# Performance work log

Measured on AMD Instinct MI355X. Metric: run time of the kernel, lower is better.

Reference implementation:

```python
import jax, jax.numpy as jnp
import numpy as np

N_NODES = 50000


def _relgraphconv(x, W, Wloop, b, src, dst, etypes, n_nodes):
    # DGL RelGraphConv (regularizer=None, self_loop=True, norm=None):
    # out[i] = sum over incoming edges (j->i, rel r) of W_r @ x[j]  +  W_loop @ x[i]  +  b
    # low-mem form: transform all nodes per relation, then gather per edge.
    h_rel = jnp.einsum('ni,rio->rno', x, W)          # [R, N, out]
    msg = h_rel[etypes, src]                          # [E, out]
    agg = jax.ops.segment_sum(msg, dst, num_segments=n_nodes)  # [N, out]
    return agg + x @ Wloop + b


def setup_inputs() -> dict:
    key = jax.random.key(0)
    ks = jax.random.split(key, 12)
    N, E, n_state = N_NODES, 800000, 128
    inp = {
        'x': jax.random.normal(ks[0], (N, n_state), dtype=jnp.float32),
        'src': jax.random.randint(ks[1], (E,), 0, N, dtype=jnp.int32),
        'dst': jax.random.randint(ks[2], (E,), 0, N, dtype=jnp.int32),
        'etypes': jax.random.randint(ks[3], (E,), 0, 2, dtype=jnp.int32),
        'cell_size': jax.random.randint(ks[4], (N,), 0, 8, dtype=jnp.int32),
        'max_size': jax.random.randint(ks[5], (N,), 0, 8, dtype=jnp.int32),
        'W1': jax.random.normal(ks[6], (2, n_state, 64), dtype=jnp.float32) * 0.05,
        'loop1': jax.random.normal(ks[7], (n_state, 64), dtype=jnp.float32) * 0.05,
        'b1': jnp.zeros((64,), dtype=jnp.float32),
        'W2': jax.random.normal(ks[8], (2, 64, 64), dtype=jnp.float32) * 0.05,
        'loop2': jax.random.normal(ks[9], (64, 64), dtype=jnp.float32) * 0.05,
        'b2': jnp.zeros((64,), dtype=jnp.float32),
        'W3': jax.random.normal(ks[10], (2, 64, 2), dtype=jnp.float32) * 0.05,
        'loop3': jax.random.normal(ks[11], (64, 2), dtype=jnp.float32) * 0.05,
        'b3': jnp.zeros((2,), dtype=jnp.float32),
    }
    return inp


def reference(x, src, dst, etypes, cell_size, max_size,
              W1, loop1, b1, W2, loop2, b2, W3, loop3, b3):
    N = x.shape[0]
    h = jax.nn.relu(_relgraphconv(x, W1, loop1, b1, src, dst, etypes, N))
    h = jax.nn.relu(_relgraphconv(h, W2, loop2, b2, src, dst, etypes, N))
    h = _relgraphconv(h, W3, loop3, b3, src, dst, etypes, N)   # [N, 2]
    # action mask: col 0 = cannot upsize, col 1 = cannot downsize
    upper = cell_size >= (max_size - 1)
    lower = cell_size == 0
    mask = jnp.stack([upper, lower], axis=1)                   # [N, 2] bool
    return jnp.where(mask, h.min() - 1.0, h)
```

## Files before the change

### kernel.cpp

```cpp
#include <hip/hip_runtime.h>


#define STRIDE 64
#define BINCAP 2560

typedef unsigned short ushortT;
typedef __attribute__((ext_vector_type(8))) short short8;
typedef __attribute__((ext_vector_type(4))) float f32x4;

__device__ inline ushortT f2bf(float f) {
    union { float f; unsigned u; } v; v.f = f;
    unsigned r = v.u + 0x7FFFu + ((v.u >> 16) & 1u);
    return (ushortT)(r >> 16);
}
__device__ inline float bf2f(ushortT h) {
    union { unsigned u; float f; } v; v.u = ((unsigned)h) << 16;
    return v.f;
}

__device__ inline void atomicMinF(float* addr, float v) {
    if (v >= 0.f) atomicMin((int*)addr, __float_as_int(v));
    else          atomicMax((unsigned int*)addr, __float_as_uint(v));
}

__global__ __launch_bounds__(256) void pack_init_kernel(
    const float* __restrict__ W1, const float* __restrict__ loop1,
    const float* __restrict__ W2, const float* __restrict__ loop2,
    ushortT* __restrict__ BP1, ushortT* __restrict__ BP2,
    int* __restrict__ bincnt, float* __restrict__ minval,
    int* __restrict__ done, int NBINS) {
    int g = (int)blockIdx.x * 256 + (int)threadIdx.x;
    if (g < NBINS) bincnt[g] = 0;
    if (g == 0) { *(int*)minval = 0x7f7f7f7f; *done = 0; }
    if (g < 3072) {
        int l = g & 63, ks = (g >> 6) & 3, ct = g >> 8;
        int c = ct * 16 + (l & 15);
        int mat = c >> 6, cc = c & 63;
        int kbase = ks * 32 + (l >> 4) * 8;
        ushortT* dstp = BP1 + (size_t)g * 8;
#pragma unroll
        for (int j = 0; j < 8; ++j) {
            int k = kbase + j;
            float v = (mat < 2) ? W1[((size_t)mat * 128 + k) * 64 + cc]
                                : loop1[(size_t)k * 64 + cc];
            dstp[j] = f2bf(v);
        }
    } else {
        int s = g - 3072;
        int l = s & 63, ks = (s >> 6) & 1, ct = s >> 7;
        int c = ct * 16 + (l & 15);
        int mat = c >> 6, cc = c & 63;
        int kbase = ks * 32 + (l >> 4) * 8;
        ushortT* dstp = BP2 + (size_t)s * 8;
#pragma unroll
        for (int j = 0; j < 8; ++j) {
            int k = kbase + j;
            float v = (mat < 2) ? W2[((size_t)mat * 64 + k) * 64 + cc]
                                : loop2[(size_t)k * 64 + cc];
            dstp[j] = f2bf(v);
        }
    }
}

__global__ __launch_bounds__(256) void k1_kernel(
    const float* __restrict__ x, const ushortT* __restrict__ BP1,
    const float* __restrict__ b1,
    ushortT* __restrict__ hrelb, ushortT* __restrict__ H1b,
    const int* __restrict__ src, const int* __restrict__ dst,
    const int* __restrict__ et, int* __restrict__ bincnt, int2* __restrict__ binbuf,
    int N, int E, int NBINS, int NBA) {
    __shared__ int hist[512];
    __shared__ int gbase[512];
    __shared__ ushortT rnk[4096];

    const int t = (int)threadIdx.x;

    if ((int)blockIdx.x < NBA) {
        for (int i = t; i < NBINS; i += 256) hist[i] = 0;
        __syncthreads();
        const int base = (int)blockIdx.x * 4096;
#pragma unroll
        for (int i = 0; i < 16; ++i) {
            int e = base + t + i * 256;
            if (e < E) {
                int bb = dst[e] >> 7;
                rnk[t + i * 256] = (ushortT)atomicAdd(&hist[bb], 1);
            }
        }
        __syncthreads();
        for (int i = t; i < NBINS; i += 256) {
            int h = hist[i];
            gbase[i] = h ? atomicAdd(&bincnt[i], h) : 0;
        }
        __syncthreads();
#pragma unroll
        for (int i = 0; i < 16; ++i) {
            int e = base + t + i * 256;
            if (e < E) {
                int dd = dst[e];
                int bb = dd >> 7;
                int v = et[e] * N + src[e];
                int pos = gbase[bb] + (int)rnk[t + i * 256];
                if (pos < BINCAP)
                    binbuf[(size_t)bb * BINCAP + pos] = make_int2(dd, v);
            }
        }
        return;
    }
    const int w = t >> 6, lane = t & 63;
    const int rowbase = (((int)blockIdx.x - NBA) * 4 + w) * 16;
    const int m = lane & 15, quad = lane >> 4;
    const int nclamp = min(rowbase + m, N - 1);

    short8 a[4];
    const float* xp = x + (size_t)nclamp * 128 + quad * 8;
#pragma unroll
    for (int ks = 0; ks < 4; ++ks) {
        float4 g0 = *(const float4*)(xp + ks * 32);
        float4 g1 = *(const float4*)(xp + ks * 32 + 4);
        a[ks][0] = (short)f2bf(g0.x); a[ks][1] = (short)f2bf(g0.y);
        a[ks][2] = (short)f2bf(g0.z); a[ks][3] = (short)f2bf(g0.w);
        a[ks][4] = (short)f2bf(g1.x); a[ks][5] = (short)f2bf(g1.y);
        a[ks][6] = (short)f2bf(g1.z); a[ks][7] = (short)f2bf(g1.w);
    }

    f32x4 acc[12];
#pragma unroll
    for (int ct = 0; ct < 12; ++ct) acc[ct] = (f32x4){0.f, 0.f, 0.f, 0.f};

#pragma unroll
    for (int ks = 0; ks < 4; ++ks) {
#pragma unroll
        for (int ct = 0; ct < 12; ++ct) {
            short8 b = *(const short8*)&BP1[((size_t)(ct * 4 + ks) * 64 + lane) * 8];
            acc[ct] = __builtin_amdgcn_mfma_f32_16x16x32_bf16(a[ks], b, acc[ct], 0, 0, 0);
        }
    }

    const int node0 = rowbase + quad * 4;
#pragma unroll
    for (int ct = 0; ct < 12; ++ct) {
        int c = ct * 16 + m;
        int mat = c >> 6, cc = c & 63;
        float bias = (mat == 2) ? b1[cc] : 0.f;
#pragma unroll
        for (int j = 0; j < 4; ++j) {
            int n = node0 + j;
            if (n < N) {
                float v = acc[ct][j] + bias;
                if (mat < 2) hrelb[((size_t)mat * N + n) * 64 + cc] = f2bf(v);
                else         H1b[(size_t)n * 64 + cc] = f2bf(v);
            }
        }
    }
}

__global__ __launch_bounds__(512, 4) void ag2_kernel(
    const ushortT* __restrict__ hrelb, const ushortT* __restrict__ H1b,
    const ushortT* __restrict__ BP2, const float* __restrict__ b2,
    const int* __restrict__ bincnt, const int2* __restrict__ binbuf,
    int* __restrict__ eidx, int* __restrict__ cnt,
    ushortT* __restrict__ hrel2b, ushortT* __restrict__ H2b, int N) {
    __shared__ int lcnt[64];
    __shared__ int lidx[64][STRIDE];
    __shared__ __align__(16) ushortT Hs[64][72];

    const int t = (int)threadIdx.x;
    const int B = (int)blockIdx.x;
    const int nodeBase = B * 64;
    const int bin = B >> 1;

    if (t < 64) lcnt[t] = 0;
    __syncthreads();

    const int cb = min(bincnt[bin], BINCAP);
    const int2* buf = binbuf + (size_t)bin * BINCAP;
    for (int i = t; i < cb; i += 512) {
        int2 rec = buf[i];
        int local = rec.x - nodeBase;
        if ((unsigned)local < 64u) {
            int r = atomicAdd(&lcnt[local], 1);
            if (r < STRIDE) {
                lidx[local][r] = rec.y;
                eidx[(size_t)rec.x * STRIDE + r] = rec.y;
            }
        }
    }
    __syncthreads();
    if (t < 64) {
        int c = min(lcnt[t], STRIDE);
        lcnt[t] = c;
        int node = nodeBase + t;
        if (node < N) cnt[node] = c;
    }
    __syncthreads();

    const int w = t >> 6, lane = t & 63;

    for (int i = 0; i < 8; ++i) {
        int local = w * 8 + i;
        int node = nodeBase + local;
        if (node >= N) { Hs[local][lane] = 0; continue; }
        int deg = lcnt[local];
        float acc = bf2f(H1b[(size_t)node * 64 + lane]);
        int j = 0;
        for (; j + 7 < deg; j += 8) {
            float v[8];
#pragma unroll
            for (int q = 0; q < 8; ++q) {
                int id = lidx[local][j + q];
                v[q] = bf2f(hrelb[(size_t)id * 64 + lane]);
            }
            acc += ((v[0] + v[1]) + (v[2] + v[3])) + ((v[4] + v[5]) + (v[6] + v[7]));
        }
        for (; j < deg; ++j)
            acc += bf2f(hrelb[(size_t)lidx[local][j] * 64 + lane]);
        Hs[local][lane] = f2bf(fmaxf(acc, 0.f));
    }
    __syncthreads();

    const int rt = w & 3, h = w >> 2;
    const int m = lane & 15, quad = lane >> 4;
    short8 a[2];
#pragma unroll
    for (int ks = 0; ks < 2; ++ks)
        a[ks] = *(const short8*)&Hs[rt * 16 + m][quad * 8 + ks * 32];

    f32x4 acc[6];
#pragma unroll
    for (int c6 = 0; c6 < 6; ++c6) acc[c6] = (f32x4){0.f, 0.f, 0.f, 0.f};

#pragma unroll
    for (int ks = 0; ks < 2; ++ks) {
#pragma unroll
        for (int c6 = 0; c6 < 6; ++c6) {
            int ct = h * 6 + c6;
            short8 b = *(const short8*)&BP2[((size_t)(ct * 2 + ks) * 64 + lane) * 8];
            acc[c6] = __builtin_amdgcn_mfma_f32_16x16x32_bf16(a[ks], b, acc[c6], 0, 0, 0);
        }
    }

    const int node0 = nodeBase + rt * 16 + quad * 4;
#pragma unroll
    for (int c6 = 0; c6 < 6; ++c6) {
        int ct = h * 6 + c6;
        int c = ct * 16 + m;
        int mat = c >> 6, cc = c & 63;
        float bias = (mat == 2) ? b2[cc] : 0.f;
#pragma unroll
        for (int j = 0; j < 4; ++j) {
            int n = node0 + j;
            if (n < N) {
                float v = acc[c6][j] + bias;
                if (mat < 2) hrel2b[((size_t)mat * N + n) * 64 + cc] = f2bf(v);
                else         H2b[(size_t)n * 64 + cc] = f2bf(v);
            }
        }
    }
}

__global__ void k3_kernel(const ushortT* __restrict__ hrel2b, const ushortT* __restrict__ H2b,
                          const int* __restrict__ eidx, const int* __restrict__ cnt,
                          const float* __restrict__ W3, const float* __restrict__ loop3,
                          const float* __restrict__ b3,
                          float* __restrict__ hrel3, float* __restrict__ H3, int N) {
    int node = (int)blockIdx.x * 4 + ((int)threadIdx.x >> 6);
    if (node >= N) return;
    int lane = (int)threadIdx.x & 63;
    int deg = cnt[node];
    int my = (lane < deg) ? eidx[(size_t)node * STRIDE + lane] : 0;
    float acc = bf2f(H2b[(size_t)node * 64 + lane]);
    int j = 0;
    for (; j + 7 < deg; j += 8) {
        int id[8];
        float v[8];
#pragma unroll
        for (int q = 0; q < 8; ++q) id[q] = __shfl(my, j + q, 64);
#pragma unroll
        for (int q = 0; q < 8; ++q) v[q] = bf2f(hrel2b[(size_t)id[q] * 64 + lane]);
        acc += ((v[0] + v[1]) + (v[2] + v[3])) + ((v[4] + v[5]) + (v[6] + v[7]));
    }
    for (; j < deg; ++j)
        acc += bf2f(hrel2b[(size_t)__shfl(my, j, 64) * 64 + lane]);
    float xk = fmaxf(acc, 0.f);
    float p[6];
    p[0] = xk * W3[lane * 2 + 0];
    p[1] = xk * W3[lane * 2 + 1];
    p[2] = xk * W3[(64 + lane) * 2 + 0];
    p[3] = xk * W3[(64 + lane) * 2 + 1];
    p[4] = xk * loop3[lane * 2 + 0];
    p[5] = xk * loop3[lane * 2 + 1];
#pragma unroll
    for (int mm = 32; mm >= 1; mm >>= 1) {
#pragma unroll
        for (int q = 0; q < 6; ++q) p[q] += __shfl_xor(p[q], mm, 64);
    }
    if (lane == 0) {
        hrel3[(size_t)node * 2 + 0] = p[0];
        hrel3[(size_t)node * 2 + 1] = p[1];
        hrel3[((size_t)N + node) * 2 + 0] = p[2];
        hrel3[((size_t)N + node) * 2 + 1] = p[3];
        H3[(size_t)node * 2 + 0] = p[4] + b3[0];
        H3[(size_t)node * 2 + 1] = p[5] + b3[1];
    }
}

__global__ __launch_bounds__(256) void a3m_mask_kernel(
    const float* __restrict__ hrel3, const int* __restrict__ eidx,
    const int* __restrict__ cnt, const float* __restrict__ H3,
    const int* __restrict__ cs, const int* __restrict__ ms,
    float* __restrict__ minval, int* __restrict__ done,
    float* __restrict__ out, int N) {
    const int t = (int)threadIdx.x;
    const int n = (int)blockIdx.x * 256 + t;
    float a0 = 0.f, a1 = 0.f;
    float v = 3.4e38f;
    if (n < N) {
        a0 = H3[n * 2 + 0]; a1 = H3[n * 2 + 1];
        int deg = cnt[n];
        const int* row = &eidx[(size_t)n * STRIDE];
        int j = 0;
        for (; j + 3 < deg; j += 4) {
            int i0 = row[j], i1 = row[j + 1], i2 = row[j + 2], i3 = row[j + 3];
            float2 q0 = *(const float2*)&hrel3[(size_t)i0 * 2];
            float2 q1 = *(const float2*)&hrel3[(size_t)i1 * 2];
            float2 q2 = *(const float2*)&hrel3[(size_t)i2 * 2];
            float2 q3 = *(const float2*)&hrel3[(size_t)i3 * 2];
            a0 += (q0.x + q1.x) + (q2.x + q3.x);
            a1 += (q0.y + q1.y) + (q2.y + q3.y);
        }
        for (; j < deg; ++j) {
            float2 q = *(const float2*)&hrel3[(size_t)row[j] * 2];
            a0 += q.x; a1 += q.y;
        }
        v = fminf(a0, a1);
    }
#pragma unroll
    for (int mm = 32; mm >= 1; mm >>= 1) v = fminf(v, __shfl_xor(v, mm, 64));
    __shared__ float s[4];
    __shared__ float gm;
    if ((t & 63) == 0) s[t >> 6] = v;
    __syncthreads();
    if (t == 0) {
        atomicMinF(minval, fminf(fminf(s[0], s[1]), fminf(s[2], s[3])));
        __threadfence();
        atomicAdd(done, 1);
        while (atomicAdd(done, 0) < (int)gridDim.x)
            __builtin_amdgcn_s_sleep(2);
        gm = atomicAdd(minval, 0.0f);
    }
    __syncthreads();
    if (n < N) {
        float mn = gm - 1.0f;
        bool up = cs[n] >= ms[n] - 1;
        bool lo = cs[n] == 0;
        out[n * 2 + 0] = up ? mn : a0;
        out[n * 2 + 1] = lo ? mn : a1;
    }
}

extern "C" void kernel_launch(void* const* d_in, const int* in_sizes, int n_in,
                              void* d_out, int out_size, void* d_ws, size_t ws_size,
                              hipStream_t stream) {
    const float* x     = (const float*)d_in[0];
    const int* src     = (const int*)d_in[1];
    const int* dst     = (const int*)d_in[2];
    const int* etypes  = (const int*)d_in[3];
    const int* cellsz  = (const int*)d_in[4];
    const int* maxsz   = (const int*)d_in[5];
    const float* W1    = (const float*)d_in[6];
    const float* loop1 = (const float*)d_in[7];
    const float* b1    = (const float*)d_in[8];
    const float* W2    = (const float*)d_in[9];
    const float* loop2 = (const float*)d_in[10];
    const float* b2    = (const float*)d_in[11];
    const float* W3    = (const float*)d_in[12];
    const float* loop3 = (const float*)d_in[13];
    const float* b3    = (const float*)d_in[14];
    float* out = (float*)d_out;

    const int N = in_sizes[0] / 128;
    const int E = in_sizes[1];

    char* p = (char*)d_ws;
    auto alloc = [&](size_t bytes) -> void* {
        void* r = (void*)p;
        p += ((bytes + 255) / 256) * 256;
        return r;
    };
    ushortT* hrelb  = (ushortT*)alloc((size_t)2 * N * 64 * 2);
    ushortT* H1b    = (ushortT*)alloc((size_t)N * 64 * 2);
    ushortT* hrel2b = (ushortT*)alloc((size_t)2 * N * 64 * 2);
    ushortT* H2b    = (ushortT*)alloc((size_t)N * 64 * 2);
    float* hrel3    = (float*)alloc((size_t)2 * N * 2 * 4);
    float* H3       = (float*)alloc((size_t)N * 2 * 4);
    int* cnt        = (int*)alloc((size_t)N * 4);
    int* eidx       = (int*)alloc((size_t)N * STRIDE * 4);
    ushortT* BP1    = (ushortT*)alloc((size_t)3072 * 8 * 2);
    ushortT* BP2    = (ushortT*)alloc((size_t)1536 * 8 * 2);
    float* minval   = (float*)alloc(4);
    int* done       = (int*)alloc(4);

    const int NBINS = (N + 127) >> 7;
    int* bincnt     = (int*)alloc((size_t)NBINS * 4);
    int2* binbuf    = (int2*)alloc((size_t)NBINS * BINCAP * 8);
    (void)ws_size; (void)n_in; (void)out_size;

    const int NB_N   = (N + 255) / 256;
    const int NTILES = (N + 63) / 64;
    const int NB_W   = (N + 3) / 4;
    const int NBA    = (E + 4095) / 4096;
    const int NB_AG  = (N + 63) / 64;

    pack_init_kernel<<<18, 256, 0, stream>>>(
        W1, loop1, W2, loop2, BP1, BP2, bincnt, minval, done, NBINS);

    k1_kernel<<<NBA + NTILES, 256, 0, stream>>>(
        x, BP1, b1, hrelb, H1b,
        src, dst, etypes, bincnt, binbuf, N, E, NBINS, NBA);

    ag2_kernel<<<NB_AG, 512, 0, stream>>>(
        hrelb, H1b, BP2, b2, bincnt, binbuf, eidx, cnt, hrel2b, H2b, N);

    k3_kernel<<<NB_W, 256, 0, stream>>>(hrel2b, H2b, eidx, cnt, W3, loop3, b3,
                                        hrel3, H3, N);

    a3m_mask_kernel<<<NB_N, 256, 0, stream>>>(hrel3, eidx, cnt, H3,
                                              cellsz, maxsz, minval, done, out, N);
}
```

Baseline: 219.1 us.

## Reorder layer-2 to aggregate-then-transform using split-by-relation sums and fused GEMM

Result: slower. 231.0 us (+5.4%).

```diff
diff --git a/kernel.cpp b/kernel.cpp
--- a/kernel.cpp
+++ b/kernel.cpp
@@ -26,7 +26,7 @@
 __global__ __launch_bounds__(256) void pack_init_kernel(
     const float* __restrict__ W1, const float* __restrict__ loop1,
     const float* __restrict__ W2, const float* __restrict__ loop2,
-    ushortT* __restrict__ BP1, ushortT* __restrict__ BP2,
+    ushortT* __restrict__ BP1, ushortT* __restrict__ BP2p,
     int* __restrict__ bincnt, float* __restrict__ minval,
     int* __restrict__ done, int NBINS) {
     int g = (int)blockIdx.x * 256 + (int)threadIdx.x;
@@ -47,16 +47,15 @@
         }
     } else {
         int s = g - 3072;
-        int l = s & 63, ks = (s >> 6) & 1, ct = s >> 7;
+        int l = s & 63, ks = (s >> 6) % 6, ct = s / 384;
         int c = ct * 16 + (l & 15);
-        int mat = c >> 6, cc = c & 63;
         int kbase = ks * 32 + (l >> 4) * 8;
-        ushortT* dstp = BP2 + (size_t)s * 8;
+        ushortT* dstp = BP2p + (size_t)s * 8;
 #pragma unroll
         for (int j = 0; j < 8; ++j) {
             int k = kbase + j;
-            float v = (mat < 2) ? W2[((size_t)mat * 64 + k) * 64 + cc]
-                                : loop2[(size_t)k * 64 + cc];
+            float v = (k < 128) ? W2[(size_t)k * 64 + c]
+                                : loop2[(size_t)(k - 128) * 64 + c];
             dstp[j] = f2bf(v);
         }
     }
@@ -155,15 +154,13 @@
     }
 }
 
-__global__ __launch_bounds__(512, 4) void ag2_kernel(
-    const ushortT* __restrict__ hrelb, const ushortT* __restrict__ H1b,
-    const ushortT* __restrict__ BP2, const float* __restrict__ b2,
+__global__ __launch_bounds__(512, 4) void ag1_kernel(
+    const ushortT* __restrict__ hrelb,
     const int* __restrict__ bincnt, const int2* __restrict__ binbuf,
     int* __restrict__ eidx, int* __restrict__ cnt,
-    ushortT* __restrict__ hrel2b, ushortT* __restrict__ H2b, int N) {
+    ushortT* __restrict__ H1b, int N) {
     __shared__ int lcnt[64];
     __shared__ int lidx[64][STRIDE];
-    __shared__ __align__(16) ushortT Hs[64][72];
 
     const int t = (int)threadIdx.x;
     const int B = (int)blockIdx.x;
@@ -196,11 +193,10 @@
     __syncthreads();
 
     const int w = t >> 6, lane = t & 63;
-
     for (int i = 0; i < 8; ++i) {
         int local = w * 8 + i;
         int node = nodeBase + local;
-        if (node >= N) { Hs[local][lane] = 0; continue; }
+        if (node >= N) continue;
         int deg = lcnt[local];
         float acc = bf2f(H1b[(size_t)node * 64 + lane]);
         int j = 0;
@@ -215,74 +211,99 @@
         }
         for (; j < deg; ++j)
             acc += bf2f(hrelb[(size_t)lidx[local][j] * 64 + lane]);
-        Hs[local][lane] = f2bf(fmaxf(acc, 0.f));
+        H1b[(size_t)node * 64 + lane] = f2bf(fmaxf(acc, 0.f));
+    }
+}
+
+__global__ __launch_bounds__(512, 4) void ag2p_kernel(
+    const ushortT* __restrict__ H1b, const ushortT* __restrict__ BP2p,
+    const float* __restrict__ b2,
+    const int* __restrict__ eidx, const int* __restrict__ cnt,
+    ushortT* __restrict__ H2b, int N) {
+    __shared__ __align__(16) ushortT As[64 * 200];
+
+    const int t = (int)threadIdx.x;
+    const int nodeBase = (int)blockIdx.x * 64;
+    const int w = t >> 6, lane = t & 63;
+
+    for (int i = 0; i < 8; ++i) {
+        const int local = w * 8 + i;
+        const int node = nodeBase + local;
+        float a0 = 0.f, a1 = 0.f;
+        ushortT selfb = 0;
+        if (node < N) {
+            const int deg = cnt[node];
+            int my = eidx[(size_t)node * STRIDE + lane];
+            selfb = H1b[(size_t)node * 64 + lane];
+            int j = 0;
+            for (; j + 7 < deg; j += 8) {
+                int vv[8];
+                float vl[8];
+#pragma unroll
+                for (int q = 0; q < 8; ++q) vv[q] = __shfl(my, j + q, 64);
+#pragma unroll
+                for (int q = 0; q < 8; ++q) {
+                    int s = (vv[q] >= N) ? vv[q] - N : vv[q];
+                    vl[q] = bf2f(H1b[(size_t)s * 64 + lane]);
+                }
+#pragma unroll
+                for (int q = 0; q < 8; ++q) {
+                    bool r = vv[q] >= N;
+                    a0 += r ? 0.f : vl[q];
+                    a1 += r ? vl[q] : 0.f;
+                }
+            }
+            for (; j < deg; ++j) {
+                int v = __shfl(my, j, 64);
+                bool r = v >= N;
+                float val = bf2f(H1b[(size_t)(r ? v - N : v) * 64 + lane]);
+                a0 += r ? 0.f : val;
+                a1 += r ? val : 0.f;
+            }
+        }
+        As[local * 200 + lane]       = f2bf(a0);
+        As[local * 200 + 64 + lane]  = f2bf(a1);
+        As[local * 200 + 128 + lane] = selfb;
     }
     __syncthreads();
 
     const int rt = w & 3, h = w >> 2;
     const int m = lane & 15, quad = lane >> 4;
-    short8 a[2];
-#pragma unroll
-    for (int ks = 0; ks < 2; ++ks)
-        a[ks] = *(const short8*)&Hs[rt * 16 + m][quad * 8 + ks * 32];
-
-    f32x4 acc[6];
-#pragma unroll
-    for (int c6 = 0; c6 < 6; ++c6) acc[c6] = (f32x4){0.f, 0.f, 0.f, 0.f};
-
-#pragma unroll
-    for (int ks = 0; ks < 2; ++ks) {
-#pragma unroll
-        for (int c6 = 0; c6 < 6; ++c6) {
-            int ct = h * 6 + c6;
-            short8 b = *(const short8*)&BP2[((size_t)(ct * 2 + ks) * 64 + lane) * 8];
-            acc[c6] = __builtin_amdgcn_mfma_f32_16x16x32_bf16(a[ks], b, acc[c6], 0, 0, 0);
-        }
-    }
-
+    f32x4 acc2[2];
+    acc2[0] = (f32x4){0.f, 0.f, 0.f, 0.f};
+    acc2[1] = (f32x4){0.f, 0.f, 0.f, 0.f};
+#pragma unroll
+    for (int ks = 0; ks < 6; ++ks) {
+        short8 a = *(const short8*)&As[(rt * 16 + m) * 200 + quad * 8 + ks * 32];
+#pragma unroll
+        for (int c2 = 0; c2 < 2; ++c2) {
+            int ct = h * 2 + c2;
+            short8 b = *(const short8*)&BP2p[((size_t)(ct * 6 + ks) * 64 + lane) * 8];
+            acc2[c2] = __builtin_amdgcn_mfma_f32_16x16x32_bf16(a, b, acc2[c2], 0, 0, 0);
+        }
+    }
     const int node0 = nodeBase + rt * 16 + quad * 4;
 #pragma unroll
-    for (int c6 = 0; c6 < 6; ++c6) {
-        int ct = h * 6 + c6;
-        int c = ct * 16 + m;
-        int mat = c >> 6, cc = c & 63;
-        float bias = (mat == 2) ? b2[cc] : 0.f;
+    for (int c2 = 0; c2 < 2; ++c2) {
+        int c = (h * 2 + c2) * 16 + m;
+        float bias = b2[c];
 #pragma unroll
         for (int j = 0; j < 4; ++j) {
             int n = node0 + j;
-            if (n < N) {
-                float v = acc[c6][j] + bias;
-                if (mat < 2) hrel2b[((size_t)mat * N + n) * 64 + cc] = f2bf(v);
-                else         H2b[(size_t)n * 64 + cc] = f2bf(v);
-            }
-        }
-    }
-}
-
-__global__ void k3_kernel(const ushortT* __restrict__ hrel2b, const ushortT* __restrict__ H2b,
-                          const int* __restrict__ eidx, const int* __restrict__ cnt,
-                          const float* __restrict__ W3, const float* __restrict__ loop3,
-                          const float* __restrict__ b3,
-                          float* __restrict__ hrel3, float* __restrict__ H3, int N) {
+            if (n < N)
+                H2b[(size_t)n * 64 + c] = f2bf(fmaxf(acc2[c2][j] + bias, 0.f));
+        }
+    }
+}
+
+__global__ void k3p_kernel(const ushortT* __restrict__ H2b,
+                           const float* __restrict__ W3, const float* __restrict__ loop3,
+                           const float* __restrict__ b3,
+                           float* __restrict__ hrel3, float* __restrict__ H3, int N) {
     int node = (int)blockIdx.x * 4 + ((int)threadIdx.x >> 6);
     if (node >= N) return;
     int lane = (int)threadIdx.x & 63;
-    int deg = cnt[node];
-    int my = (lane < deg) ? eidx[(size_t)node * STRIDE + lane] : 0;
-    float acc = bf2f(H2b[(size_t)node * 64 + lane]);
-    int j = 0;
-    for (; j + 7 < deg; j += 8) {
-        int id[8];
-        float v[8];
-#pragma unroll
-        for (int q = 0; q < 8; ++q) id[q] = __shfl(my, j + q, 64);
-#pragma unroll
-        for (int q = 0; q < 8; ++q) v[q] = bf2f(hrel2b[(size_t)id[q] * 64 + lane]);
-        acc += ((v[0] + v[1]) + (v[2] + v[3])) + ((v[4] + v[5]) + (v[6] + v[7]));
-    }
-    for (; j < deg; ++j)
-        acc += bf2f(hrel2b[(size_t)__shfl(my, j, 64) * 64 + lane]);
-    float xk = fmaxf(acc, 0.f);
+    float xk = bf2f(H2b[(size_t)node * 64 + lane]);
     float p[6];
     p[0] = xk * W3[lane * 2 + 0];
     p[1] = xk * W3[lane * 2 + 1];
@@ -390,14 +411,13 @@
     };
     ushortT* hrelb  = (ushortT*)alloc((size_t)2 * N * 64 * 2);
     ushortT* H1b    = (ushortT*)alloc((size_t)N * 64 * 2);
-    ushortT* hrel2b = (ushortT*)alloc((size_t)2 * N * 64 * 2);
     ushortT* H2b    = (ushortT*)alloc((size_t)N * 64 * 2);
     float* hrel3    = (float*)alloc((size_t)2 * N * 2 * 4);
     float* H3       = (float*)alloc((size_t)N * 2 * 4);
     int* cnt        = (int*)alloc((size_t)N * 4);
     int* eidx       = (int*)alloc((size_t)N * STRIDE * 4);
     ushortT* BP1    = (ushortT*)alloc((size_t)3072 * 8 * 2);
-    ushortT* BP2    = (ushortT*)alloc((size_t)1536 * 8 * 2);
+    ushortT* BP2p   = (ushortT*)alloc((size_t)1536 * 8 * 2);
     float* minval   = (float*)alloc(4);
     int* done       = (int*)alloc(4);
 
@@ -413,17 +433,19 @@
     const int NB_AG  = (N + 63) / 64;
 
     pack_init_kernel<<<18, 256, 0, stream>>>(
-        W1, loop1, W2, loop2, BP1, BP2, bincnt, minval, done, NBINS);
+        W1, loop1, W2, loop2, BP1, BP2p, bincnt, minval, done, NBINS);
 
     k1_kernel<<<NBA + NTILES, 256, 0, stream>>>(
         x, BP1, b1, hrelb, H1b,
         src, dst, etypes, bincnt, binbuf, N, E, NBINS, NBA);
 
-    ag2_kernel<<<NB_AG, 512, 0, stream>>>(
-        hrelb, H1b, BP2, b2, bincnt, binbuf, eidx, cnt, hrel2b, H2b, N);
-
-    k3_kernel<<<NB_W, 256, 0, stream>>>(hrel2b, H2b, eidx, cnt, W3, loop3, b3,
-                                        hrel3, H3, N);
+    ag1_kernel<<<NB_AG, 512, 0, stream>>>(
+        hrelb, bincnt, binbuf, eidx, cnt, H1b, N);
+
+    ag2p_kernel<<<NB_AG, 512, 0, stream>>>(
+        H1b, BP2p, b2, eidx, cnt, H2b, N);
+
+    k3p_kernel<<<NB_W, 256, 0, stream>>>(H2b, W3, loop3, b3, hrel3, H3, N);
 
     a3m_mask_kernel<<<NB_N, 256, 0, stream>>>(hrel3, eidx, cnt, H3,
                                               cellsz, maxsz, minval, done, out, N);
```
